# Kernel tuning notes

Hardware: AMD Instinct MI355X
Metric: run time of the kernel (lower is better)

## Reference

```python
import jax, jax.numpy as jnp
import numpy as np

D_MODEL = 1024
N_HEADS = 16
HEAD_DIM = D_MODEL // N_HEADS


def setup_inputs() -> dict:
    key = jax.random.key(0)
    k_x, k_qkv, k_proj = jax.random.split(key, 3)
    x = jax.random.normal(k_x, (2, 2048, D_MODEL), dtype=jnp.float32)
    # flax nnx.Linear kernels: shape (in_features, out_features), lecun_normal-ish scale
    w_qkv = jax.random.normal(k_qkv, (D_MODEL, 3 * D_MODEL), dtype=jnp.float32) / np.sqrt(D_MODEL)
    w_proj = jax.random.normal(k_proj, (D_MODEL, D_MODEL), dtype=jnp.float32) / np.sqrt(D_MODEL)
    return {"x": x, "w_qkv": w_qkv, "w_proj": w_proj}


def reference(x, w_qkv, w_proj):
    bsz, seq_len, d_model = x.shape
    qkv = x @ w_qkv  # (B, T, 3*D)
    q, k, v = jnp.split(qkv, 3, axis=-1)
    q = q.reshape(bsz, seq_len, N_HEADS, HEAD_DIM)
    k = k.reshape(bsz, seq_len, N_HEADS, HEAD_DIM)
    v = v.reshape(bsz, seq_len, N_HEADS, HEAD_DIM)
    scale = jnp.sqrt(jnp.asarray(HEAD_DIM, dtype=x.dtype))
    attn_logits = jnp.einsum('bthd,bshd->bhts', q / scale, k)  # (B, H, T, T)
    attn_weights = jax.nn.softmax(attn_logits, axis=-1)
    attn_out = jnp.einsum('bhts,bshd->bthd', attn_weights, v)
    attn_out = attn_out.reshape(bsz, seq_len, d_model)
    return attn_out @ w_proj
```

## Files before the change

kernel.cpp:

```cpp
#include <hip/hip_runtime.h>
#include <hip/hip_bf16.h>
#include <cmath>

#define D_MODEL 1024
#define NH 16
#define HD 64
#define BSZ 2
#define SEQ 2048
#define MTOT (BSZ * SEQ)

typedef _Float16 f16x8 __attribute__((ext_vector_type(8)));
typedef __fp16   fp16x2 __attribute__((ext_vector_type(2)));
typedef float    f32x4  __attribute__((ext_vector_type(4)));
typedef float    f32x16 __attribute__((ext_vector_type(16)));
typedef unsigned int uivec2 __attribute__((ext_vector_type(2)));

#define QSCALE 0.18033688011112042f

__device__ __forceinline__ ushort f2h(float x) {
    union { _Float16 h; ushort u; } cv;
    cv.h = (_Float16)x;
    return cv.u;
}
__device__ __forceinline__ uint pkh(float a, float b) {
    union { fp16x2 h; uint u; } cv;
    cv.h = __builtin_amdgcn_cvt_pkrtz(a, b);
    return cv.u;
}
__device__ __forceinline__ float fexp2(float x) {
    float r; asm("v_exp_f32 %0, %1" : "=v"(r) : "v"(x)); return r;
}
__device__ __forceinline__ float fmax3(float a, float b, float c) {
    return fmaxf(fmaxf(a, b), c);
}
__device__ __forceinline__ void gload_lds16(const ushort* g, ushort* l) {
    __builtin_amdgcn_global_load_lds(
        (const __attribute__((address_space(1))) void*)g,
        (__attribute__((address_space(3))) void*)l, 16, 0, 0);
}

__global__ __launch_bounds__(256)
void cast8(const float* __restrict__ in, ushort* __restrict__ out, int n)
{
    const int i = (blockIdx.x * 256 + threadIdx.x) * 8;
    if (i >= n) return;
    float4 a = *(const float4*)(in + i);
    float4 b = *(const float4*)(in + i + 4);
    alignas(16) ushort h8[8];
    h8[0] = f2h(a.x); h8[1] = f2h(a.y); h8[2] = f2h(a.z); h8[3] = f2h(a.w);
    h8[4] = f2h(b.x); h8[5] = f2h(b.y); h8[6] = f2h(b.z); h8[7] = f2h(b.w);
    *(uint4*)(out + i) = *(const uint4*)h8;
}

__global__ __launch_bounds__(256)
void transpose_cast2(const float* __restrict__ A, const float* __restrict__ B,
                     ushort* __restrict__ At, ushort* __restrict__ Bt)
{
    __shared__ float tile[32][33];
    const int z = blockIdx.z;
    const float* in = (z < 3) ? A : B;
    ushort* out     = (z < 3) ? At : Bt;
    const int C     = (z < 3) ? 3 * D_MODEL : D_MODEL;
    const int cb    = (z < 3) ? z * 32 + blockIdx.x : blockIdx.x;
    const int R = D_MODEL;
    const int t  = threadIdx.x;
    const int r0 = blockIdx.y * 32, c0 = cb * 32;
    const int tr = t >> 5, tc = t & 31;
#pragma unroll
    for (int s = 0; s < 4; ++s)
        tile[tr + 8 * s][tc] = in[(size_t)(r0 + tr + 8 * s) * C + c0 + tc];
    __syncthreads();
#pragma unroll
    for (int s = 0; s < 4; ++s)
        out[(size_t)(c0 + tr + 8 * s) * R + r0 + tc] = f2h(tile[tc][tr + 8 * s]);
}

template <int MODE>
__global__ __launch_bounds__(256)
void gemm_mfma(const ushort* __restrict__ A, const ushort* __restrict__ Bt,
               float* __restrict__ outp,
               ushort* __restrict__ Qw, ushort* __restrict__ Kw,
               ushort* __restrict__ Vw, int N)
{
    __shared__ ushort As[128 * 64];
    __shared__ ushort Bs[128 * 64];

    const int t  = threadIdx.x;
    const int w  = t >> 6;
    const int l  = t & 63;
    const int lr = l & 15;
    const int lg = l >> 4;
    const int wr = w >> 1, wc = w & 1;
    const int m0 = blockIdx.y * 128, n0 = blockIdx.x * 128;

    const int srow = l >> 3;
    const int scol = (l & 7) * 8;

    const ushort* Ab = A  + (size_t)m0 * 1024;
    const ushort* Bb = Bt + (size_t)n0 * 1024;

    f32x4 acc[4][4];
#pragma unroll
    for (int i = 0; i < 4; ++i)
#pragma unroll
        for (int j = 0; j < 4; ++j) acc[i][j] = (f32x4){0.f, 0.f, 0.f, 0.f};

    for (int k0 = 0; k0 < 1024; k0 += 64) {
#pragma unroll
        for (int i = 0; i < 4; ++i) {
            const int r8 = (w * 4 + i) * 8;
            gload_lds16(Ab + (size_t)(r8 + srow) * 1024 + k0 + scol, &As[r8 * 64]);
            gload_lds16(Bb + (size_t)(r8 + srow) * 1024 + k0 + scol, &Bs[r8 * 64]);
        }
        __syncthreads();

#pragma unroll
        for (int kk = 0; kk < 2; ++kk) {
            f16x8 af[4], bf[4];
#pragma unroll
            for (int m = 0; m < 4; ++m)
                af[m] = *(const f16x8*)&As[(wr * 64 + m * 16 + lr) * 64 + kk * 32 + lg * 8];
#pragma unroll
            for (int n = 0; n < 4; ++n)
                bf[n] = *(const f16x8*)&Bs[(wc * 64 + n * 16 + lr) * 64 + kk * 32 + lg * 8];
#pragma unroll
            for (int m = 0; m < 4; ++m)
#pragma unroll
                for (int n = 0; n < 4; ++n)
                    acc[m][n] = __builtin_amdgcn_mfma_f32_16x16x32_f16(
                        af[m], bf[n], acc[m][n], 0, 0, 0);
        }
        __syncthreads();
    }

    if (MODE == 1) {
#pragma unroll
        for (int mf = 0; mf < 4; ++mf) {
            const int row = m0 + wr * 64 + mf * 16 + lg * 4;
#pragma unroll
            for (int nf = 0; nf < 4; ++nf) {
                const int col = n0 + wc * 64 + nf * 16 + lr;
#pragma unroll
                for (int i = 0; i < 4; ++i)
                    outp[(size_t)(row + i) * N + col] = acc[mf][nf][i];
            }
        }
    } else {
#pragma unroll
        for (int mf = 0; mf < 4; ++mf) {
            const int row = m0 + wr * 64 + mf * 16 + lg * 4;
            const int b   = row >> 11;
            const int tt0 = row & (SEQ - 1);
#pragma unroll
            for (int nf = 0; nf < 4; ++nf) {
                const int col   = n0 + wc * 64 + nf * 16 + lr;
                const int which = col >> 10;
                const int h     = (col >> 6) & 15;
                const int d     = col & 63;
                ushort* dst = (which == 0) ? Qw : (which == 1) ? Kw : Vw;
                const float sc = (which == 0) ? QSCALE : 1.0f;
#pragma unroll
                for (int i = 0; i < 4; ++i)
                    dst[((size_t)(b * NH + h) * SEQ + tt0 + i) * HD + d] =
                        f2h(acc[mf][nf][i] * sc);
            }
        }
    }
}

__global__ __launch_bounds__(512, 4)
void attn_mfma6(const ushort* __restrict__ Qw, const ushort* __restrict__ Kw,
                const ushort* __restrict__ Vw, ushort* __restrict__ AO)
{
    __shared__ ushort KsAll[2][2][64 * 64];
    __shared__ ushort VtAll[2][2][64 * 64];

    const int t    = threadIdx.x;
    const int w    = t >> 6;
    const int l    = t & 63;
    const int q    = l & 31;
    const int hi   = l >> 5;
    const int half = w >> 2;
    const int ww   = w & 3;

    const int bh = blockIdx.y;
    const int q0 = blockIdx.x * 128 + ww * 32;
    const int kbase = half * (SEQ / 2);
    const int NT = (SEQ / 2) / 64;

    const ushort* Qp = Qw + (size_t)bh * SEQ * HD;
    const ushort* Kp = Kw + (size_t)bh * SEQ * HD;
    const ushort* Vp = Vw + (size_t)bh * SEQ * HD;

    ushort (*Ks)[64 * 64] = KsAll[half];
    ushort (*Vt)[64 * 64] = VtAll[half];

    f16x8 qf[4];
#pragma unroll
    for (int kc = 0; kc < 4; ++kc)
        qf[kc] = *(const f16x8*)(Qp + (size_t)(q0 + q) * HD + kc * 16 + hi * 8);

    f32x16 oacc[2];
#pragma unroll
    for (int db = 0; db < 2; ++db)
#pragma unroll
        for (int r = 0; r < 16; ++r) oacc[db][r] = 0.f;
    float m_run = -3.0e38f, l_run = 0.f;

    auto stageK = [&](int buf, int k0) {
#pragma unroll
        for (int s = 0; s < 2; ++s) {
            const int c    = ww * 64 + l + 256 * s;
            const int row  = c >> 3;
            const int unit = (c & 7) ^ (row & 7);
            gload_lds16(Kp + (size_t)(k0 + row) * HD + unit * 8,
                        &Ks[buf][(ww * 64 + 256 * s) * 8]);
        }
    };
    const int vkey = l;
    auto loadV = [&](int k0, uint4& r0, uint4& r1) {
        r0 = *(const uint4*)(Vp + (size_t)(k0 + vkey) * HD + ww * 8);
        r1 = *(const uint4*)(Vp + (size_t)(k0 + vkey) * HD + (ww + 4) * 8);
    };
    auto writeV = [&](int buf, uint4 r0, uint4 r1) {
        alignas(16) ushort e8[8];
        *(uint4*)e8 = r0;
#pragma unroll
        for (int i = 0; i < 8; ++i) {
            const int d = ww * 8 + i;
            *(ushort*)((char*)Vt[buf] + (d * 128 + ((vkey * 2) ^ (i << 4)))) = e8[i];
        }
        *(uint4*)e8 = r1;
#pragma unroll
        for (int i = 0; i < 8; ++i) {
            const int d = (ww + 4) * 8 + i;
            *(ushort*)((char*)Vt[buf] + (d * 128 + ((vkey * 2) ^ (i << 4)))) = e8[i];
        }
    };

    {
        uint4 r0, r1;
        stageK(0, kbase);
        loadV(kbase, r0, r1);
        writeV(0, r0, r1);
    }
    __syncthreads();

    int cur = 0;
    for (int kt = 0; kt < NT; ++kt) {
        const bool pf = (kt + 1 < NT);
        uint4 vr0, vr1;
        if (pf) {
            stageK(cur ^ 1, kbase + (kt + 1) * 64);
            loadV(kbase + (kt + 1) * 64, vr0, vr1);
        }

        f32x16 sacc[2];
        __builtin_amdgcn_s_setprio(1);
#pragma unroll
        for (int kb = 0; kb < 2; ++kb) {
            f32x16 a;
#pragma unroll
            for (int r = 0; r < 16; ++r) a[r] = 0.f;
            const int row = kb * 32 + q;
            const int swz = (row & 7) << 4;
#pragma unroll
            for (int kc = 0; kc < 4; ++kc) {
                f16x8 kf = *(const f16x8*)(
                    (const char*)Ks[cur] + row * 128 + ((kc * 32 + hi * 16) ^ swz));
                a = __builtin_amdgcn_mfma_f32_32x32x16_f16(kf, qf[kc], a, 0, 0, 0);
            }
            sacc[kb] = a;
        }
        __builtin_amdgcn_s_setprio(0);

        float p0 = fmax3(fmaxf(sacc[0][0], sacc[1][0]),
                         fmaxf(sacc[0][1], sacc[1][1]),
                         fmaxf(sacc[0][2], sacc[1][2]));
        float p1 = fmax3(fmaxf(sacc[0][3], sacc[1][3]),
                         fmaxf(sacc[0][4], sacc[1][4]),
                         fmaxf(sacc[0][5], sacc[1][5]));
        float p2 = fmax3(fmaxf(sacc[0][6], sacc[1][6]),
                         fmaxf(sacc[0][7], sacc[1][7]),
                         fmaxf(sacc[0][8], sacc[1][8]));
        float p3 = fmax3(fmaxf(sacc[0][9], sacc[1][9]),
                         fmaxf(sacc[0][10], sacc[1][10]),
                         fmaxf(sacc[0][11], sacc[1][11]));
        float p4 = fmax3(fmaxf(sacc[0][12], sacc[1][12]),
                         fmaxf(sacc[0][13], sacc[1][13]),
                         fmaxf(sacc[0][14], sacc[1][14]));
        float p5 = fmaxf(sacc[0][15], sacc[1][15]);
        float mx = fmaxf(fmax3(p0, p1, p2), fmax3(p3, p4, p5));
        mx = fmaxf(mx, __shfl_xor(mx, 32));

        if (__any(mx > m_run + 8.0f)) {
            const float m_new = fmaxf(m_run, mx);
            const float scale = fexp2(m_run - m_new);
            m_run = m_new;
            l_run *= scale;
#pragma unroll
            for (int db = 0; db < 2; ++db)
#pragma unroll
                for (int r = 0; r < 16; ++r) oacc[db][r] *= scale;
        }

#pragma unroll
        for (int kb = 0; kb < 2; ++kb)
#pragma unroll
            for (int r = 0; r < 16; ++r)
                sacc[kb][r] = fexp2(sacc[kb][r] - m_run);

        float ts[16];
#pragma unroll
        for (int r = 0; r < 16; ++r) ts[r] = sacc[0][r] + sacc[1][r];
#pragma unroll
        for (int s = 8; s > 0; s >>= 1)
#pragma unroll
            for (int r = 0; r < 8; ++r)
                if (r < s) ts[r] += ts[r + s];
        l_run += ts[0] + __shfl_xor(ts[0], 32);

        f16x8 pfrag[4];
#pragma unroll
        for (int kb = 0; kb < 2; ++kb)
#pragma unroll
            for (int lc = 0; lc < 2; ++lc) {
                const int rb = lc * 8;
                uint a = pkh(sacc[kb][rb + 0], sacc[kb][rb + 1]);
                uint b = pkh(sacc[kb][rb + 2], sacc[kb][rb + 3]);
                uint c = pkh(sacc[kb][rb + 4], sacc[kb][rb + 5]);
                uint d = pkh(sacc[kb][rb + 6], sacc[kb][rb + 7]);
                uivec2 r0 = __builtin_amdgcn_permlane32_swap(a, c, false, false);
                uivec2 r1 = __builtin_amdgcn_permlane32_swap(b, d, false, false);
                union { uint u[4]; f16x8 v; } f;
                f.u[0] = r0.x;
                f.u[1] = r1.x;
                f.u[2] = r0.y;
                f.u[3] = r1.y;
                pfrag[kb * 2 + lc] = f.v;
            }

        __builtin_amdgcn_s_setprio(1);
#pragma unroll
        for (int db = 0; db < 2; ++db) {
            const int row = db * 32 + q;
            const int swz = (row & 7) << 4;
#pragma unroll
            for (int kc = 0; kc < 4; ++kc) {
                f16x8 vf = *(const f16x8*)(
                    (const char*)Vt[cur] + row * 128 + ((kc * 32 + hi * 16) ^ swz));
                oacc[db] = __builtin_amdgcn_mfma_f32_32x32x16_f16(
                    vf, pfrag[kc], oacc[db], 0, 0, 0);
            }
        }
        __builtin_amdgcn_s_setprio(0);

        if (pf) writeV(cur ^ 1, vr0, vr1);
        __syncthreads();
        cur ^= 1;
    }

    float* oex = (float*)KsAll;
    float* mex = (float*)VtAll;
    float* lex = mex + 256;

    if (half == 1) {
        mex[ww * 64 + l] = m_run;
        lex[ww * 64 + l] = l_run;
#pragma unroll
        for (int db = 0; db < 2; ++db)
#pragma unroll
            for (int r = 0; r < 16; ++r)
                oex[(((ww * 2 + db) * 16) + r) * 64 + l] = oacc[db][r];
    }
    __syncthreads();
    if (half == 0) {
        const float m2 = mex[ww * 64 + l];
        const float l2 = lex[ww * 64 + l];
        const float mf = fmaxf(m_run, m2);
        float w1 = fexp2(m_run - mf), w2 = fexp2(m2 - mf);
        const float inv = 1.f / (l_run * w1 + l2 * w2);
        w1 *= inv; w2 *= inv;

        const int b = bh >> 4, h = bh & 15;
        ushort* orow = AO + ((size_t)(b * SEQ) + q0 + q) * D_MODEL + h * HD;
#pragma unroll
        for (int db = 0; db < 2; ++db)
#pragma unroll
            for (int g = 0; g < 4; ++g) {
                const int d = db * 32 + g * 8 + hi * 4;
                alignas(8) ushort e4[4];
#pragma unroll
                for (int i = 0; i < 4; ++i) {
                    const float o2 = oex[(((ww * 2 + db) * 16) + g * 4 + i) * 64 + l];
                    e4[i] = f2h(oacc[db][g * 4 + i] * w1 + o2 * w2);
                }
                *(uint2*)(orow + d) = *(const uint2*)e4;
            }
    }
}

extern "C" void kernel_launch(void* const* d_in, const int* in_sizes, int n_in,
                              void* d_out, int out_size, void* d_ws, size_t ws_size,
                              hipStream_t stream)
{
    const float* x      = (const float*)d_in[0];
    const float* w_qkv  = (const float*)d_in[1];
    const float* w_proj = (const float*)d_in[2];
    float* out = (float*)d_out;

    ushort* Xh  = (ushort*)d_ws;
    ushort* WqT = Xh  + (size_t)MTOT * D_MODEL;
    ushort* WpT = WqT + (size_t)3 * D_MODEL * D_MODEL;
    ushort* Qw  = WpT + (size_t)D_MODEL * D_MODEL;
    ushort* Kw  = Qw  + (size_t)MTOT * D_MODEL;
    ushort* Vw  = Kw  + (size_t)MTOT * D_MODEL;
    ushort* AOh = Vw  + (size_t)MTOT * D_MODEL;

    dim3 blk(256);

    cast8<<<dim3(MTOT * D_MODEL / (8 * 256)), blk, 0, stream>>>(x, Xh, MTOT * D_MODEL);
    transpose_cast2<<<dim3(32, 32, 4), blk, 0, stream>>>(w_qkv, w_proj, WqT, WpT);

    gemm_mfma<0><<<dim3(3 * D_MODEL / 128, MTOT / 128), blk, 0, stream>>>(
        Xh, WqT, nullptr, Qw, Kw, Vw, 3 * D_MODEL);

    attn_mfma6<<<dim3(SEQ / 128, BSZ * NH), dim3(512), 0, stream>>>(Qw, Kw, Vw, AOh);

    gemm_mfma<1><<<dim3(D_MODEL / 128, MTOT / 128), blk, 0, stream>>>(
        AOh, WpT, out, nullptr, nullptr, nullptr, D_MODEL);
}
```

Before: 148.3 us.

## Write V pre-transposed from QKV GEMM and stage it via async LDS loads

The QKV projection epilogue now writes V in a head-dim-major (transposed) global layout, packing four consecutive sequence positions into one 8-byte store. The attention kernel can then stage V tiles with the same direct global-to-LDS swizzled loads used for K. This removes the per-element scalar LDS transpose writes and the register staging of V inside the attention loop. The cost moves to the GEMM epilogue, whose V stores are strided by SEQ, so its write coalescing changes.

```diff
diff --git a/kernel.cpp b/kernel.cpp
--- a/kernel.cpp
+++ b/kernel.cpp
@@ -157,20 +157,28 @@
                 const int which = col >> 10;
                 const int h     = (col >> 6) & 15;
                 const int d     = col & 63;
-                ushort* dst = (which == 0) ? Qw : (which == 1) ? Kw : Vw;
-                const float sc = (which == 0) ? QSCALE : 1.0f;
-#pragma unroll
-                for (int i = 0; i < 4; ++i)
-                    dst[((size_t)(b * NH + h) * SEQ + tt0 + i) * HD + d] =
-                        f2h(acc[mf][nf][i] * sc);
+                if (which == 2) {
+                    ushort* p = Vw + (((size_t)(b * NH + h) * HD + d) * SEQ) + tt0;
+                    alignas(8) ushort e4[4];
+#pragma unroll
+                    for (int i = 0; i < 4; ++i) e4[i] = f2h(acc[mf][nf][i]);
+                    *(uint2*)p = *(const uint2*)e4;
+                } else {
+                    ushort* dst = (which == 0) ? Qw : Kw;
+                    const float sc = (which == 0) ? QSCALE : 1.0f;
+#pragma unroll
+                    for (int i = 0; i < 4; ++i)
+                        dst[((size_t)(b * NH + h) * SEQ + tt0 + i) * HD + d] =
+                            f2h(acc[mf][nf][i] * sc);
+                }
             }
         }
     }
 }
 
 __global__ __launch_bounds__(512, 4)
-void attn_mfma6(const ushort* __restrict__ Qw, const ushort* __restrict__ Kw,
-                const ushort* __restrict__ Vw, ushort* __restrict__ AO)
+void attn_mfma7(const ushort* __restrict__ Qw, const ushort* __restrict__ Kw,
+                const ushort* __restrict__ Vtg, ushort* __restrict__ AO)
 {
     __shared__ ushort KsAll[2][2][64 * 64];
     __shared__ ushort VtAll[2][2][64 * 64];
@@ -188,9 +196,9 @@
     const int kbase = half * (SEQ / 2);
     const int NT = (SEQ / 2) / 64;
 
-    const ushort* Qp = Qw + (size_t)bh * SEQ * HD;
-    const ushort* Kp = Kw + (size_t)bh * SEQ * HD;
-    const ushort* Vp = Vw + (size_t)bh * SEQ * HD;
+    const ushort* Qp = Qw  + (size_t)bh * SEQ * HD;
+    const ushort* Kp = Kw  + (size_t)bh * SEQ * HD;
+    const ushort* Vp = Vtg + (size_t)bh * HD * SEQ;
 
     ushort (*Ks)[64 * 64] = KsAll[half];
     ushort (*Vt)[64 * 64] = VtAll[half];
@@ -217,42 +225,26 @@
                         &Ks[buf][(ww * 64 + 256 * s) * 8]);
         }
     };
-    const int vkey = l;
-    auto loadV = [&](int k0, uint4& r0, uint4& r1) {
-        r0 = *(const uint4*)(Vp + (size_t)(k0 + vkey) * HD + ww * 8);
-        r1 = *(const uint4*)(Vp + (size_t)(k0 + vkey) * HD + (ww + 4) * 8);
+    auto stageV = [&](int buf, int k0) {
+#pragma unroll
+        for (int s = 0; s < 2; ++s) {
+            const int c    = ww * 64 + l + 256 * s;
+            const int row  = c >> 3;
+            const int unit = (c & 7) ^ (row & 7);
+            gload_lds16(Vp + (size_t)row * SEQ + k0 + unit * 8,
+                        &Vt[buf][(ww * 64 + 256 * s) * 8]);
+        }
     };
-    auto writeV = [&](int buf, uint4 r0, uint4 r1) {
-        alignas(16) ushort e8[8];
-        *(uint4*)e8 = r0;
-#pragma unroll
-        for (int i = 0; i < 8; ++i) {
-            const int d = ww * 8 + i;
-            *(ushort*)((char*)Vt[buf] + (d * 128 + ((vkey * 2) ^ (i << 4)))) = e8[i];
-        }
-        *(uint4*)e8 = r1;
-#pragma unroll
-        for (int i = 0; i < 8; ++i) {
-            const int d = (ww + 4) * 8 + i;
-            *(ushort*)((char*)Vt[buf] + (d * 128 + ((vkey * 2) ^ (i << 4)))) = e8[i];
-        }
-    };
-
-    {
-        uint4 r0, r1;
-        stageK(0, kbase);
-        loadV(kbase, r0, r1);
-        writeV(0, r0, r1);
-    }
+
+    stageK(0, kbase);
+    stageV(0, kbase);
     __syncthreads();
 
     int cur = 0;
     for (int kt = 0; kt < NT; ++kt) {
-        const bool pf = (kt + 1 < NT);
-        uint4 vr0, vr1;
-        if (pf) {
+        if (kt + 1 < NT) {
             stageK(cur ^ 1, kbase + (kt + 1) * 64);
-            loadV(kbase + (kt + 1) * 64, vr0, vr1);
+            stageV(cur ^ 1, kbase + (kt + 1) * 64);
         }
 
         f32x16 sacc[2];
@@ -355,7 +347,6 @@
         }
         __builtin_amdgcn_s_setprio(0);
 
-        if (pf) writeV(cur ^ 1, vr0, vr1);
         __syncthreads();
         cur ^= 1;
     }
@@ -414,8 +405,8 @@
     ushort* WpT = WqT + (size_t)3 * D_MODEL * D_MODEL;
     ushort* Qw  = WpT + (size_t)D_MODEL * D_MODEL;
     ushort* Kw  = Qw  + (size_t)MTOT * D_MODEL;
-    ushort* Vw  = Kw  + (size_t)MTOT * D_MODEL;
-    ushort* AOh = Vw  + (size_t)MTOT * D_MODEL;
+    ushort* Vt  = Kw  + (size_t)MTOT * D_MODEL;
+    ushort* AOh = Vt  + (size_t)MTOT * D_MODEL;
 
     dim3 blk(256);
 
@@ -423,9 +414,9 @@
     transpose_cast2<<<dim3(32, 32, 4), blk, 0, stream>>>(w_qkv, w_proj, WqT, WpT);
 
     gemm_mfma<0><<<dim3(3 * D_MODEL / 128, MTOT / 128), blk, 0, stream>>>(
-        Xh, WqT, nullptr, Qw, Kw, Vw, 3 * D_MODEL);
-
-    attn_mfma6<<<dim3(SEQ / 128, BSZ * NH), dim3(512), 0, stream>>>(Qw, Kw, Vw, AOh);
+        Xh, WqT, nullptr, Qw, Kw, Vt, 3 * D_MODEL);
+
+    attn_mfma7<<<dim3(SEQ / 128, BSZ * NH), dim3(512), 0, stream>>>(Qw, Kw, Vt, AOh);
 
     gemm_mfma<1><<<dim3(D_MODEL / 128, MTOT / 128), blk, 0, stream>>>(
         AOh, WpT, out, nullptr, nullptr, nullptr, D_MODEL);
```

Result: faster. 142.5 us (-3.9%).
